# Performance work log

Hardware: AMD Instinct MI355X
Metric: run time of the kernel (lower is better)

## Reference

```python
import jax, jax.numpy as jnp
import numpy as np

B, P, D = 256, 128, 768        # batch, property slots per sample, encoder hidden dim
E = 64                          # num_properties (number of adapter heads)
H = 256                         # adapter_hidden_dim
H2 = H // 2
O = 2                           # output_dim
LN_EPS = 1e-5
RES_W_ADPT, RES_W_BASE = 0.7, 0.3


def setup_inputs() -> dict:
    key = jax.random.key(0)
    ks = jax.random.split(key, 12)
    hidden_states = jax.random.normal(ks[0], (B, P, D), dtype=jnp.float32)
    base_output = jax.random.normal(ks[1], (B, P, O), dtype=jnp.float32)
    properties = jax.random.randint(ks[2], (B, P), 0, E, dtype=jnp.int64)
    mask = (jax.random.uniform(ks[3], (B, P)) > 0.1).astype(jnp.float32)
    # Stacked per-head adapter parameters (LayerNorm + 3 Linears per head)
    ln_g = jnp.ones((E, D), dtype=jnp.float32)
    ln_b = jnp.zeros((E, D), dtype=jnp.float32)
    W1 = jax.random.normal(ks[4], (E, D, H), dtype=jnp.float32) * (1.0 / np.sqrt(D))
    b1 = jnp.zeros((E, H), dtype=jnp.float32)
    W2 = jax.random.normal(ks[5], (E, H, H2), dtype=jnp.float32) * (1.0 / np.sqrt(H))
    b2 = jnp.zeros((E, H2), dtype=jnp.float32)
    W3 = jax.random.normal(ks[6], (E, H2, O), dtype=jnp.float32) * 0.01  # init std=0.01 per source
    b3 = jnp.zeros((E, O), dtype=jnp.float32)
    return {
        "hidden_states": hidden_states, "base_output": base_output,
        "properties": properties, "mask": mask,
        "ln_g": ln_g, "ln_b": ln_b, "W1": W1, "b1": b1,
        "W2": W2, "b2": b2, "W3": W3, "b3": b3,
    }


def reference(hidden_states, base_output, properties, mask,
              ln_g, ln_b, W1, b1, W2, b2, W3, b3):
    b, p, d = hidden_states.shape
    o = W3.shape[-1]
    x = hidden_states.reshape(-1, d)                        # [N, D]
    # LayerNorm statistics are head-independent; only gamma/beta differ per head
    mu = jnp.mean(x, axis=-1, keepdims=True)
    var = jnp.mean((x - mu) ** 2, axis=-1, keepdims=True)
    xhat = (x - mu) * jax.lax.rsqrt(var + LN_EPS)           # [N, D]
    flat_p = properties.reshape(-1)                         # [N]
    flat_m = mask.reshape(-1)                               # [N]

    def body(acc, inp):
        idx, g, bt, w1, bb1, w2, bb2, w3, bb3 = inp
        h = jax.nn.relu((xhat * g + bt) @ w1 + bb1)         # [N, H]  (dropout = identity in eval)
        h = jax.nn.relu(h @ w2 + bb2)                       # [N, H2]
        out = h @ w3 + bb3                                  # [N, O]
        sel = (flat_p == idx) & (flat_m > 0)
        return jnp.where(sel[:, None], out, acc), None

    e = W1.shape[0]
    acc0 = jnp.zeros((b * p, o), dtype=x.dtype)
    acc, _ = jax.lax.scan(
        body, acc0,
        (jnp.arange(e), ln_g, ln_b, W1, b1, W2, b2, W3, b3))
    out = acc.reshape(b, p, o)
    out = RES_W_ADPT * out + RES_W_BASE * base_output       # use_residual=True
    return out * mask[..., None]
```

## Files before the change

kernel.cpp:

```cpp
#include <hip/hip_runtime.h>
#include <stdint.h>

typedef unsigned short u16;
typedef unsigned int   u32;

#define NTOK   32768
#define GD     768
#define GH     256
#define GH2    128
#define GE     64

typedef __bf16 bf16x8 __attribute__((ext_vector_type(8)));
typedef float  f32x4  __attribute__((ext_vector_type(4)));
union Frag { uint4 u; bf16x8 b; };

__device__ __forceinline__ float bf2f(u16 h) {
  union { u32 u; float f; } v; v.u = ((u32)h) << 16; return v.f;
}
__device__ __forceinline__ u16 f2bf(float f) {
  union { float f; u32 u; } v; v.f = f;
  u32 r = (v.u + 0x7fffu + ((v.u >> 16) & 1u)) >> 16;
  return (u16)r;
}

__device__ __forceinline__ void async16(void* lds, const void* g) {
  __builtin_amdgcn_global_load_lds(
      (const __attribute__((address_space(1))) void*)g,
      (__attribute__((address_space(3))) void*)lds, 16, 0, 0);
}

__device__ __forceinline__ int getProp(const int* p32, int t, int is64) {
  return is64 ? p32[2 * t] : p32[t];
}

static const size_t OFF_Y    = 0;
static const size_t OFF_W1T  = 50331648;
static const size_t OFF_W2T  = 75497472;
static const size_t OFF_TOK  = 79691776;
static const size_t OFF_META = 79822848;

__global__ void setup_kernel(const int* __restrict__ prop, const float* __restrict__ mask,
                             u32* __restrict__ outz, int* __restrict__ counts2d,
                             int* __restrict__ cursors_p, int* __restrict__ flagp) {
  __shared__ int h[GE];
  __shared__ int vOr;
  const int b = blockIdx.x;
  const int tid = threadIdx.x;
  outz[b * 512 + tid] = 0u;
  outz[b * 512 + 256 + tid] = 0u;
  if (b < 4) cursors_p[b * 256 + tid] = 0;
  if (tid < GE) h[tid] = 0;
  if (tid == 0) vOr = 0;
  __syncthreads();
  int v = prop[2 * tid + 1] | prop[2 * (tid + 256) + 1];
  if (v) atomicOr(&vOr, 1);
  __syncthreads();
  const int is64 = (vOr == 0) ? 1 : 0;
  if (b == 0 && tid == 0) *flagp = is64;
  const int t = b * 256 + tid;
  if (mask[t] > 0.f) atomicAdd(&h[getProp(prop, t, is64)], 1);
  __syncthreads();
  if (tid < GE) counts2d[b * GE + tid] = h[tid];
}

__global__ void transpose_w1(const float* __restrict__ in, u16* __restrict__ out) {
  __shared__ u16 tl[64][260];
  const int bid = blockIdx.x;
  const int e  = bid / 12, r = bid % 12;
  const int d0 = (r / 4) * 256, h0 = (r % 4) * 64;
  const int tid = threadIdx.x;
  const size_t inMat = (size_t)e * GD * GH;
  const size_t outMat = (size_t)e * GH * GD;
  const int h_l = (tid & 15) * 4, d_l = tid >> 4;
#pragma unroll
  for (int dd = 0; dd < 16; ++dd) {
    const int d = d_l + dd * 16;
    float4 v = *(const float4*)(in + inMat + (size_t)(d0 + d) * GH + h0 + h_l);
    tl[h_l + 0][d] = f2bf(v.x);
    tl[h_l + 1][d] = f2bf(v.y);
    tl[h_l + 2][d] = f2bf(v.z);
    tl[h_l + 3][d] = f2bf(v.w);
  }
  __syncthreads();
  const int wv = tid >> 6, ln = tid & 63;
#pragma unroll
  for (int hh = 0; hh < 16; ++hh) {
    const int h = wv * 16 + hh;
    *(uint2*)(out + outMat + (size_t)(h0 + h) * GD + d0 + ln * 4) =
        *(const uint2*)&tl[h][ln * 4];
  }
}

__global__ void transpose_kernel(const float* __restrict__ in, u16* __restrict__ out,
                                 int R, int C, int tilesC) {
  __shared__ u16 tile[32][33];
  const int tilesPerMat = (R >> 5) * tilesC;
  const int e  = blockIdx.x / tilesPerMat;
  const int t  = blockIdx.x % tilesPerMat;
  const int tr = t / tilesC, tc = t % tilesC;
  const size_t mat = (size_t)e * R * C;
  const int tx = threadIdx.x & 31, ty = threadIdx.x >> 5;
  const int r0 = tr * 32, c0 = tc * 32;
#pragma unroll
  for (int i = 0; i < 32; i += 8)
    tile[ty + i][tx] = f2bf(in[mat + (size_t)(r0 + ty + i) * C + c0 + tx]);
  __syncthreads();
#pragma unroll
  for (int i = 0; i < 32; i += 8)
    out[mat + (size_t)(c0 + ty + i) * R + r0 + tx] = tile[tx][ty + i];
}

__global__ void ln_kernel(const float* __restrict__ hs, const float* __restrict__ g,
                          const float* __restrict__ bta, const int* __restrict__ prop,
                          u16* __restrict__ y, const int* __restrict__ flag) {
  const int wv = threadIdx.x >> 6, ln = threadIdx.x & 63;
  const int t = blockIdx.x * 4 + wv;
  const float* x = hs + (size_t)t * GD;
  float v[12];
  float s = 0.f, sq = 0.f;
#pragma unroll
  for (int c = 0; c < 3; ++c) {
    float4 u = *(const float4*)(x + c * 256 + ln * 4);
    v[c*4+0] = u.x; v[c*4+1] = u.y; v[c*4+2] = u.z; v[c*4+3] = u.w;
    s  += u.x + u.y + u.z + u.w;
    sq += u.x*u.x + u.y*u.y + u.z*u.z + u.w*u.w;
  }
#pragma unroll
  for (int d = 1; d < 64; d <<= 1) { s += __shfl_xor(s, d); sq += __shfl_xor(sq, d); }
  const float mu = s * (1.f / 768.f);
  const float rstd = rsqrtf(sq * (1.f / 768.f) - mu * mu + 1e-5f);
  const int p = getProp(prop, t, *flag);
  const float* gp = g + (size_t)p * GD;
  const float* bp = bta + (size_t)p * GD;
  u16* yp = y + (size_t)t * GD;
#pragma unroll
  for (int c = 0; c < 3; ++c) {
    float4 ug = *(const float4*)(gp + c * 256 + ln * 4);
    float4 ub = *(const float4*)(bp + c * 256 + ln * 4);
    float y0 = (v[c*4+0] - mu) * rstd * ug.x + ub.x;
    float y1 = (v[c*4+1] - mu) * rstd * ug.y + ub.y;
    float y2 = (v[c*4+2] - mu) * rstd * ug.z + ub.z;
    float y3 = (v[c*4+3] - mu) * rstd * ug.w + ub.w;
    uint2 o;
    o.x = (u32)f2bf(y0) | ((u32)f2bf(y1) << 16);
    o.y = (u32)f2bf(y2) | ((u32)f2bf(y3) << 16);
    *(uint2*)(yp + c * 256 + ln * 4) = o;
  }
}

__global__ void scan_kernel(const int* __restrict__ counts2d, int* __restrict__ offsets,
                            int* __restrict__ tileHead, int* __restrict__ tileRow,
                            int* __restrict__ nTilesPtr) {
  const int e = threadIdx.x;
  int c = 0;
  for (int b = 0; b < 128; ++b) c += counts2d[b * GE + e];
  int inc = c;
#pragma unroll
  for (int d = 1; d < 64; d <<= 1) { int n = __shfl_up(inc, d); if (e >= d) inc += n; }
  const int off = inc - c;
  offsets[e] = off;
  if (e == 63) offsets[64] = inc;
  int ntile = (c + 63) >> 6;
  int inct = ntile;
#pragma unroll
  for (int d = 1; d < 64; d <<= 1) { int n = __shfl_up(inct, d); if (e >= d) inct += n; }
  const int tb = inct - ntile;
  for (int j = 0; j < ntile; ++j) { tileHead[tb + j] = e; tileRow[tb + j] = off + j * 64; }
  if (e == 63) *nTilesPtr = inct;
}

__global__ void scatter_kernel(const int* __restrict__ prop, const float* __restrict__ mask,
                               const int* __restrict__ offsets, int* __restrict__ cursors_p,
                               int* __restrict__ tokenIds, const int* __restrict__ flag) {
  __shared__ int h[GE];
  __shared__ int basebin[GE];
  const int tid = threadIdx.x;
  const int t = blockIdx.x * 256 + tid;
  if (tid < GE) h[tid] = 0;
  __syncthreads();
  int p = -1, rank = 0;
  if (mask[t] > 0.f) {
    p = getProp(prop, t, *flag);
    rank = atomicAdd(&h[p], 1);
  }
  __syncthreads();
  if (tid < GE && h[tid] > 0) basebin[tid] = atomicAdd(&cursors_p[tid * 16], h[tid]);
  __syncthreads();
  if (p >= 0) tokenIds[offsets[p] + basebin[p] + rank] = t;
}

__global__ __launch_bounds__(256, 2) void adapter_gemm(
    const u16* __restrict__ y, const u16* __restrict__ w1t, const u16* __restrict__ w2t,
    const float* __restrict__ b1, const float* __restrict__ b2,
    const float* __restrict__ w3, const float* __restrict__ b3,
    const float* __restrict__ base, const float* __restrict__ mask,
    const int* __restrict__ tokenIds, const int* __restrict__ offsets,
    const int* __restrict__ tileHead, const int* __restrict__ tileRow,
    const int* __restrict__ nTilesPtr, float* __restrict__ outp) {
  __shared__ union LU {
    struct { u16 A[2][2048]; u16 B[2][8192]; } s;
    u16 h[17408];
  } uni;
  __shared__ u16 sB2[2][4096];
  __shared__ float sBias1[256];
  __shared__ float sBias2[128];
  __shared__ float sW3[2][128];
  __shared__ float sB3[2];
  __shared__ int   sTok[64];

  const int tid  = threadIdx.x;
  const int wv   = tid >> 6;
  const int ln   = tid & 63;
  const int l15  = tid & 15;
  const int quad = (tid & 63) >> 4;
  const f32x4 vzero = {0.f, 0.f, 0.f, 0.f};
  const int nt = *nTilesPtr;

  for (int tile = blockIdx.x; tile < nt; tile += gridDim.x) {
    __syncthreads();
    const int e  = tileHead[tile];
    const int rs = tileRow[tile];
    const int nRows = min(64, offsets[e + 1] - rs);

    if (tid < 64) sTok[tid] = tokenIds[rs + min(tid, nRows - 1)];
    sBias1[tid] = b1[e * GH + tid];
    if (tid < 128) sBias2[tid] = b2[e * GH2 + tid];
    { const int k = tid >> 1, o = tid & 1; sW3[o][k] = w3[e * GH2 * 2 + k * 2 + o]; }
    if (tid < 2) sB3[tid] = b3[e * 2 + tid];
    __syncthreads();

    const u16* yrow = y + (size_t)sTok[ln] * GD;
    const u16* w1e = w1t + (size_t)e * GH * GD;
    const u16* w2e = w2t + (size_t)e * GH2 * GH;

    f32x4 acc1[4][4];
#pragma unroll
    for (int f = 0; f < 4; ++f)
#pragma unroll
      for (int g = 0; g < 4; ++g) acc1[f][g] = vzero;

    {
      async16(uni.s.A[0] + wv * 512, yrow + wv * 8);
#pragma unroll
      for (int j = 0; j < 4; ++j)
        async16(uni.s.B[0] + wv * 2048 + j * 512,
                w1e + (size_t)(j * 64 + ln) * GD + wv * 8);
    }

    for (int kt = 0; kt < 24; ++kt) {
      __syncthreads();
      if (kt + 1 < 24) {
        const int k0 = (kt + 1) * 32;
        const int par = (kt + 1) & 1;
        async16(uni.s.A[par] + wv * 512, yrow + k0 + wv * 8);
#pragma unroll
        for (int j = 0; j < 4; ++j)
          async16(uni.s.B[par] + wv * 2048 + j * 512,
                  w1e + (size_t)(j * 64 + ln) * GD + k0 + wv * 8);
      }
      const int par = kt & 1;
      Frag fa[4], fb[4];
#pragma unroll
      for (int f = 0; f < 4; ++f)
        fa[f].u = *(const uint4*)&uni.s.A[par][quad * 512 + (f * 16 + l15) * 8];
#pragma unroll
      for (int g = 0; g < 4; ++g)
        fb[g].u = *(const uint4*)&uni.s.B[par][quad * 2048 + (wv * 64 + g * 16 + l15) * 8];
#pragma unroll
      for (int f = 0; f < 4; ++f)
#pragma unroll
        for (int g = 0; g < 4; ++g)
          acc1[f][g] = __builtin_amdgcn_mfma_f32_16x16x32_bf16(fa[f].b, fb[g].b, acc1[f][g], 0, 0, 0);
    }
    __syncthreads();

#pragma unroll
    for (int j = 0; j < 2; ++j)
      async16(sB2[0] + wv * 1024 + j * 512,
              w2e + (size_t)(j * 64 + ln) * GH + wv * 8);

#pragma unroll
    for (int f = 0; f < 4; ++f)
#pragma unroll
      for (int g = 0; g < 4; ++g) {
        const int col = wv * 64 + g * 16 + l15;
        const float bias = sBias1[col];
#pragma unroll
        for (int r = 0; r < 4; ++r) {
          const int row = f * 16 + quad * 4 + r;
          uni.h[row * 264 + col] = f2bf(fmaxf(acc1[f][g][r] + bias, 0.f));
        }
      }

    f32x4 acc2[4][2];
#pragma unroll
    for (int f = 0; f < 4; ++f)
#pragma unroll
      for (int g = 0; g < 2; ++g) acc2[f][g] = vzero;

    for (int kt = 0; kt < 8; ++kt) {
      __syncthreads();
      if (kt + 1 < 8) {
        const int k0 = (kt + 1) * 32;
        const int par = (kt + 1) & 1;
#pragma unroll
        for (int j = 0; j < 2; ++j)
          async16(sB2[par] + wv * 1024 + j * 512,
                  w2e + (size_t)(j * 64 + ln) * GH + k0 + wv * 8);
      }
      const int par = kt & 1;
      Frag fa2[4], fb2[2];
#pragma unroll
      for (int f = 0; f < 4; ++f)
        fa2[f].u = *(const uint4*)&uni.h[(f * 16 + l15) * 264 + kt * 32 + quad * 8];
#pragma unroll
      for (int g = 0; g < 2; ++g)
        fb2[g].u = *(const uint4*)&sB2[par][quad * 1024 + (wv * 32 + g * 16 + l15) * 8];
#pragma unroll
      for (int f = 0; f < 4; ++f)
#pragma unroll
        for (int g = 0; g < 2; ++g)
          acc2[f][g] = __builtin_amdgcn_mfma_f32_16x16x32_bf16(fa2[f].b, fb2[g].b, acc2[f][g], 0, 0, 0);
    }
    __syncthreads();

#pragma unroll
    for (int f = 0; f < 4; ++f)
#pragma unroll
      for (int g = 0; g < 2; ++g) {
        const int col = wv * 32 + g * 16 + l15;
        const float bias = sBias2[col];
#pragma unroll
        for (int r = 0; r < 4; ++r) {
          const int row = f * 16 + quad * 4 + r;
          uni.h[row * 130 + col] = f2bf(fmaxf(acc2[f][g][r] + bias, 0.f));
        }
      }
    __syncthreads();

    const int m = tid >> 1, o = tid & 1;
    if (m < nRows) {
      float a = sB3[o];
      const u16* h2row = &uni.h[m * 130];
#pragma unroll 16
      for (int k = 0; k < 128; ++k) a += bf2f(h2row[k]) * sW3[o][k];
      const int t = sTok[m];
      const float mk = mask[t];
      const float bs = base[t * 2 + o];
      outp[t * 2 + o] = (0.7f * a + 0.3f * bs) * mk;
    }
  }
}

extern "C" void kernel_launch(void* const* d_in, const int* in_sizes, int n_in,
                              void* d_out, int out_size, void* d_ws, size_t ws_size,
                              hipStream_t stream) {
  const float* hs   = (const float*)d_in[0];
  const float* base = (const float*)d_in[1];
  const int*   prop = (const int*)d_in[2];
  const float* mask = (const float*)d_in[3];
  const float* lng  = (const float*)d_in[4];
  const float* lnb  = (const float*)d_in[5];
  const float* W1   = (const float*)d_in[6];
  const float* b1   = (const float*)d_in[7];
  const float* W2   = (const float*)d_in[8];
  const float* b2   = (const float*)d_in[9];
  const float* W3   = (const float*)d_in[10];
  const float* b3   = (const float*)d_in[11];

  char* ws = (char*)d_ws;
  u16* y    = (u16*)(ws + OFF_Y);
  u16* w1t  = (u16*)(ws + OFF_W1T);
  u16* w2t  = (u16*)(ws + OFF_W2T);
  int* tok  = (int*)(ws + OFF_TOK);
  int* meta = (int*)(ws + OFF_META);
  int* counts2d  = meta;
  int* offsets   = meta + 8192;
  int* tileHead  = meta + 8320;
  int* tileRow   = meta + 9344;
  int* nTiles    = meta + 10368;
  int* propFlag  = meta + 10369;
  int* cursors_p = meta + 10432;

  setup_kernel<<<128, 256, 0, stream>>>(prop, mask, (u32*)d_out, counts2d,
                                        cursors_p, propFlag);
  transpose_w1<<<768, 256, 0, stream>>>(W1, w1t);
  transpose_kernel<<<64 * 8 * 4, 256, 0, stream>>>(W2, w2t, GH, GH2, 4);
  ln_kernel<<<NTOK / 4, 256, 0, stream>>>(hs, lng, lnb, prop, y, propFlag);
  scan_kernel<<<1, 64, 0, stream>>>(counts2d, offsets, tileHead, tileRow, nTiles);
  scatter_kernel<<<NTOK / 256, 256, 0, stream>>>(prop, mask, offsets, cursors_p, tok, propFlag);
  adapter_gemm<<<640, 256, 0, stream>>>(y, w1t, w2t, b1, b2, W3, b3, base, mask,
                                        tok, offsets, tileHead, tileRow, nTiles,
                                        (float*)d_out);
}
```

Baseline: 283.0 us.

## Fuse LayerNorm into grouped adapter GEMM and merge prep kernels

Drops the separate LayerNorm pass that wrote a bf16 normalized copy of hidden_states. Each GEMM tile now computes per-token mean and rstd from the fp32 input and normalizes with per-head gamma/beta while staging its A operand into shared memory. The setup and both weight transposes are merged into one launch, and counts2d is stored transposed so the scan can read it with vector loads. This removes a full write and reread of the normalized activations plus several launches. In exchange the GEMM reads fp32 rows twice (once for stats, once for the operand), uses synchronous loads for A instead of async copies, and needs more shared memory, which may lower occupancy.

```diff
diff --git a/kernel.cpp b/kernel.cpp
--- a/kernel.cpp
+++ b/kernel.cpp
@@ -33,118 +33,80 @@
   return is64 ? p32[2 * t] : p32[t];
 }
 
-static const size_t OFF_Y    = 0;
-static const size_t OFF_W1T  = 50331648;
-static const size_t OFF_W2T  = 75497472;
-static const size_t OFF_TOK  = 79691776;
-static const size_t OFF_META = 79822848;
-
-__global__ void setup_kernel(const int* __restrict__ prop, const float* __restrict__ mask,
-                             u32* __restrict__ outz, int* __restrict__ counts2d,
-                             int* __restrict__ cursors_p, int* __restrict__ flagp) {
-  __shared__ int h[GE];
-  __shared__ int vOr;
+static const size_t OFF_W1T  = 0;
+static const size_t OFF_W2T  = 25165824;
+static const size_t OFF_TOK  = 29360128;
+static const size_t OFF_META = 29491200;
+
+__global__ void mega_prep(const int* __restrict__ prop, const float* __restrict__ mask,
+                          const float* __restrict__ W1, const float* __restrict__ W2,
+                          u32* __restrict__ outz, u16* __restrict__ w1t,
+                          u16* __restrict__ w2t, int* __restrict__ counts2d,
+                          int* __restrict__ cursors_p, int* __restrict__ flagp) {
+  __shared__ union SM {
+    struct { int h[GE]; int vOr; } st;
+    u16 w1[64][260];
+    u16 t32[32][33];
+  } sm;
   const int b = blockIdx.x;
   const int tid = threadIdx.x;
-  outz[b * 512 + tid] = 0u;
-  outz[b * 512 + 256 + tid] = 0u;
-  if (b < 4) cursors_p[b * 256 + tid] = 0;
-  if (tid < GE) h[tid] = 0;
-  if (tid == 0) vOr = 0;
-  __syncthreads();
-  int v = prop[2 * tid + 1] | prop[2 * (tid + 256) + 1];
-  if (v) atomicOr(&vOr, 1);
-  __syncthreads();
-  const int is64 = (vOr == 0) ? 1 : 0;
-  if (b == 0 && tid == 0) *flagp = is64;
-  const int t = b * 256 + tid;
-  if (mask[t] > 0.f) atomicAdd(&h[getProp(prop, t, is64)], 1);
-  __syncthreads();
-  if (tid < GE) counts2d[b * GE + tid] = h[tid];
-}
-
-__global__ void transpose_w1(const float* __restrict__ in, u16* __restrict__ out) {
-  __shared__ u16 tl[64][260];
-  const int bid = blockIdx.x;
-  const int e  = bid / 12, r = bid % 12;
-  const int d0 = (r / 4) * 256, h0 = (r % 4) * 64;
-  const int tid = threadIdx.x;
-  const size_t inMat = (size_t)e * GD * GH;
-  const size_t outMat = (size_t)e * GH * GD;
-  const int h_l = (tid & 15) * 4, d_l = tid >> 4;
-#pragma unroll
-  for (int dd = 0; dd < 16; ++dd) {
-    const int d = d_l + dd * 16;
-    float4 v = *(const float4*)(in + inMat + (size_t)(d0 + d) * GH + h0 + h_l);
-    tl[h_l + 0][d] = f2bf(v.x);
-    tl[h_l + 1][d] = f2bf(v.y);
-    tl[h_l + 2][d] = f2bf(v.z);
-    tl[h_l + 3][d] = f2bf(v.w);
-  }
-  __syncthreads();
-  const int wv = tid >> 6, ln = tid & 63;
-#pragma unroll
-  for (int hh = 0; hh < 16; ++hh) {
-    const int h = wv * 16 + hh;
-    *(uint2*)(out + outMat + (size_t)(h0 + h) * GD + d0 + ln * 4) =
-        *(const uint2*)&tl[h][ln * 4];
-  }
-}
-
-__global__ void transpose_kernel(const float* __restrict__ in, u16* __restrict__ out,
-                                 int R, int C, int tilesC) {
-  __shared__ u16 tile[32][33];
-  const int tilesPerMat = (R >> 5) * tilesC;
-  const int e  = blockIdx.x / tilesPerMat;
-  const int t  = blockIdx.x % tilesPerMat;
-  const int tr = t / tilesC, tc = t % tilesC;
-  const size_t mat = (size_t)e * R * C;
-  const int tx = threadIdx.x & 31, ty = threadIdx.x >> 5;
-  const int r0 = tr * 32, c0 = tc * 32;
-#pragma unroll
-  for (int i = 0; i < 32; i += 8)
-    tile[ty + i][tx] = f2bf(in[mat + (size_t)(r0 + ty + i) * C + c0 + tx]);
-  __syncthreads();
-#pragma unroll
-  for (int i = 0; i < 32; i += 8)
-    out[mat + (size_t)(c0 + ty + i) * R + r0 + tx] = tile[tx][ty + i];
-}
-
-__global__ void ln_kernel(const float* __restrict__ hs, const float* __restrict__ g,
-                          const float* __restrict__ bta, const int* __restrict__ prop,
-                          u16* __restrict__ y, const int* __restrict__ flag) {
-  const int wv = threadIdx.x >> 6, ln = threadIdx.x & 63;
-  const int t = blockIdx.x * 4 + wv;
-  const float* x = hs + (size_t)t * GD;
-  float v[12];
-  float s = 0.f, sq = 0.f;
-#pragma unroll
-  for (int c = 0; c < 3; ++c) {
-    float4 u = *(const float4*)(x + c * 256 + ln * 4);
-    v[c*4+0] = u.x; v[c*4+1] = u.y; v[c*4+2] = u.z; v[c*4+3] = u.w;
-    s  += u.x + u.y + u.z + u.w;
-    sq += u.x*u.x + u.y*u.y + u.z*u.z + u.w*u.w;
-  }
-#pragma unroll
-  for (int d = 1; d < 64; d <<= 1) { s += __shfl_xor(s, d); sq += __shfl_xor(sq, d); }
-  const float mu = s * (1.f / 768.f);
-  const float rstd = rsqrtf(sq * (1.f / 768.f) - mu * mu + 1e-5f);
-  const int p = getProp(prop, t, *flag);
-  const float* gp = g + (size_t)p * GD;
-  const float* bp = bta + (size_t)p * GD;
-  u16* yp = y + (size_t)t * GD;
-#pragma unroll
-  for (int c = 0; c < 3; ++c) {
-    float4 ug = *(const float4*)(gp + c * 256 + ln * 4);
-    float4 ub = *(const float4*)(bp + c * 256 + ln * 4);
-    float y0 = (v[c*4+0] - mu) * rstd * ug.x + ub.x;
-    float y1 = (v[c*4+1] - mu) * rstd * ug.y + ub.y;
-    float y2 = (v[c*4+2] - mu) * rstd * ug.z + ub.z;
-    float y3 = (v[c*4+3] - mu) * rstd * ug.w + ub.w;
-    uint2 o;
-    o.x = (u32)f2bf(y0) | ((u32)f2bf(y1) << 16);
-    o.y = (u32)f2bf(y2) | ((u32)f2bf(y3) << 16);
-    *(uint2*)(yp + c * 256 + ln * 4) = o;
+
+  if (b < 128) {
+    outz[b * 512 + tid] = 0u;
+    outz[b * 512 + 256 + tid] = 0u;
+    if (b < 4) cursors_p[b * 256 + tid] = 0;
+    if (tid < GE) sm.st.h[tid] = 0;
+    if (tid == 0) sm.st.vOr = 0;
+    __syncthreads();
+    int v = prop[2 * tid + 1] | prop[2 * (tid + 256) + 1];
+    if (v) atomicOr(&sm.st.vOr, 1);
+    __syncthreads();
+    const int is64 = (sm.st.vOr == 0) ? 1 : 0;
+    if (b == 0 && tid == 0) *flagp = is64;
+    const int t = b * 256 + tid;
+    if (mask[t] > 0.f) atomicAdd(&sm.st.h[getProp(prop, t, is64)], 1);
+    __syncthreads();
+    if (tid < GE) counts2d[tid * 128 + b] = sm.st.h[tid];
+  } else if (b < 896) {
+    const int bid = b - 128;
+    const int e  = bid / 12, r = bid % 12;
+    const int d0 = (r / 4) * 256, h0 = (r % 4) * 64;
+    const size_t inMat = (size_t)e * GD * GH;
+    const size_t outMat = (size_t)e * GH * GD;
+    const int h_l = (tid & 15) * 4, d_l = tid >> 4;
+#pragma unroll
+    for (int dd = 0; dd < 16; ++dd) {
+      const int d = d_l + dd * 16;
+      float4 v = *(const float4*)(W1 + inMat + (size_t)(d0 + d) * GH + h0 + h_l);
+      sm.w1[h_l + 0][d] = f2bf(v.x);
+      sm.w1[h_l + 1][d] = f2bf(v.y);
+      sm.w1[h_l + 2][d] = f2bf(v.z);
+      sm.w1[h_l + 3][d] = f2bf(v.w);
+    }
+    __syncthreads();
+    const int wv = tid >> 6, ln = tid & 63;
+#pragma unroll
+    for (int hh = 0; hh < 16; ++hh) {
+      const int h = wv * 16 + hh;
+      *(uint2*)(w1t + outMat + (size_t)(h0 + h) * GD + d0 + ln * 4) =
+          *(const uint2*)&sm.w1[h][ln * 4];
+    }
+  } else {
+    const int bid = b - 896;
+    const int R = GH, C = GH2, tilesC = 4, tilesPerMat = 32;
+    const int e  = bid / tilesPerMat;
+    const int t  = bid % tilesPerMat;
+    const int tr = t / tilesC, tc = t % tilesC;
+    const size_t mat = (size_t)e * R * C;
+    const int tx = tid & 31, ty = tid >> 5;
+    const int r0 = tr * 32, c0 = tc * 32;
+#pragma unroll
+    for (int i = 0; i < 32; i += 8)
+      sm.t32[ty + i][tx] = f2bf(W2[mat + (size_t)(r0 + ty + i) * C + c0 + tx]);
+    __syncthreads();
+#pragma unroll
+    for (int i = 0; i < 32; i += 8)
+      w2t[mat + (size_t)(c0 + ty + i) * R + r0 + tx] = sm.t32[tx][ty + i];
   }
 }
 
@@ -153,7 +115,9 @@
                             int* __restrict__ nTilesPtr) {
   const int e = threadIdx.x;
   int c = 0;
-  for (int b = 0; b < 128; ++b) c += counts2d[b * GE + e];
+  const int4* p = (const int4*)(counts2d + e * 128);
+#pragma unroll
+  for (int i = 0; i < 32; ++i) { int4 v = p[i]; c += v.x + v.y + v.z + v.w; }
   int inc = c;
 #pragma unroll
   for (int d = 1; d < 64; d <<= 1) { int n = __shfl_up(inc, d); if (e >= d) inc += n; }
@@ -190,7 +154,8 @@
 }
 
 __global__ __launch_bounds__(256, 2) void adapter_gemm(
-    const u16* __restrict__ y, const u16* __restrict__ w1t, const u16* __restrict__ w2t,
+    const float* __restrict__ hs, const float* __restrict__ lng, const float* __restrict__ lnb,
+    const u16* __restrict__ w1t, const u16* __restrict__ w2t,
     const float* __restrict__ b1, const float* __restrict__ b2,
     const float* __restrict__ w3, const float* __restrict__ b3,
     const float* __restrict__ base, const float* __restrict__ mask,
@@ -198,7 +163,14 @@
     const int* __restrict__ tileHead, const int* __restrict__ tileRow,
     const int* __restrict__ nTilesPtr, float* __restrict__ outp) {
   __shared__ union LU {
-    struct { u16 A[2][2048]; u16 B[2][8192]; } s;
+    struct {
+      u16 A[2][2048];
+      u16 B[2][8192];
+      u16 G[768];
+      u16 Bt[768];
+      float mu[64];
+      float rstd[64];
+    } s;
     u16 h[17408];
   } uni;
   __shared__ u16 sB2[2][4096];
@@ -227,11 +199,39 @@
     if (tid < 128) sBias2[tid] = b2[e * GH2 + tid];
     { const int k = tid >> 1, o = tid & 1; sW3[o][k] = w3[e * GH2 * 2 + k * 2 + o]; }
     if (tid < 2) sB3[tid] = b3[e * 2 + tid];
-    __syncthreads();
-
-    const u16* yrow = y + (size_t)sTok[ln] * GD;
+#pragma unroll
+    for (int i = 0; i < 3; ++i) {
+      const int idx = i * 256 + tid;
+      uni.s.G[idx]  = f2bf(lng[e * GD + idx]);
+      uni.s.Bt[idx] = f2bf(lnb[e * GD + idx]);
+    }
+    __syncthreads();
+
+    {
+      const int srow = tid >> 2, sj = tid & 3;
+      const float* xr = hs + (size_t)sTok[srow] * GD;
+      float s = 0.f, sq = 0.f;
+#pragma unroll
+      for (int i = 0; i < 48; ++i) {
+        float4 u = *(const float4*)(xr + i * 16 + sj * 4);
+        s  += u.x + u.y + u.z + u.w;
+        sq += u.x * u.x + u.y * u.y + u.z * u.z + u.w * u.w;
+      }
+      s += __shfl_xor(s, 1);  s += __shfl_xor(s, 2);
+      sq += __shfl_xor(sq, 1); sq += __shfl_xor(sq, 2);
+      if (sj == 0) {
+        const float m = s * (1.f / 768.f);
+        uni.s.mu[srow]   = m;
+        uni.s.rstd[srow] = rsqrtf(sq * (1.f / 768.f) - m * m + 1e-5f);
+      }
+    }
+    __syncthreads();
+
+    const float* xrow = hs + (size_t)sTok[ln] * GD;
     const u16* w1e = w1t + (size_t)e * GH * GD;
     const u16* w2e = w2t + (size_t)e * GH2 * GH;
+    const float lmu = uni.s.mu[ln];
+    const float lrs = uni.s.rstd[ln];
 
     f32x4 acc1[4][4];
 #pragma unroll
@@ -239,26 +239,44 @@
 #pragma unroll
       for (int g = 0; g < 4; ++g) acc1[f][g] = vzero;
 
-    {
-      async16(uni.s.A[0] + wv * 512, yrow + wv * 8);
-#pragma unroll
-      for (int j = 0; j < 4; ++j)
-        async16(uni.s.B[0] + wv * 2048 + j * 512,
-                w1e + (size_t)(j * 64 + ln) * GD + wv * 8);
-    }
+    float4 pa = *(const float4*)(xrow + wv * 8);
+    float4 pb = *(const float4*)(xrow + wv * 8 + 4);
+#pragma unroll
+    for (int j = 0; j < 4; ++j)
+      async16(uni.s.B[0] + wv * 2048 + j * 512,
+              w1e + (size_t)(j * 64 + ln) * GD + wv * 8);
 
     for (int kt = 0; kt < 24; ++kt) {
+      const int par = kt & 1;
+      {
+        const int kb = kt * 32 + wv * 8;
+        const uint4 gv = *(const uint4*)&uni.s.G[kb];
+        const uint4 bv = *(const uint4*)&uni.s.Bt[kb];
+        const float xn0 = (pa.x - lmu) * lrs * bf2f((u16)(gv.x & 0xffff)) + bf2f((u16)(bv.x & 0xffff));
+        const float xn1 = (pa.y - lmu) * lrs * bf2f((u16)(gv.x >> 16))    + bf2f((u16)(bv.x >> 16));
+        const float xn2 = (pa.z - lmu) * lrs * bf2f((u16)(gv.y & 0xffff)) + bf2f((u16)(bv.y & 0xffff));
+        const float xn3 = (pa.w - lmu) * lrs * bf2f((u16)(gv.y >> 16))    + bf2f((u16)(bv.y >> 16));
+        const float xn4 = (pb.x - lmu) * lrs * bf2f((u16)(gv.z & 0xffff)) + bf2f((u16)(bv.z & 0xffff));
+        const float xn5 = (pb.y - lmu) * lrs * bf2f((u16)(gv.z >> 16))    + bf2f((u16)(bv.z >> 16));
+        const float xn6 = (pb.z - lmu) * lrs * bf2f((u16)(gv.w & 0xffff)) + bf2f((u16)(bv.w & 0xffff));
+        const float xn7 = (pb.w - lmu) * lrs * bf2f((u16)(gv.w >> 16))    + bf2f((u16)(bv.w >> 16));
+        uint4 pk;
+        pk.x = (u32)f2bf(xn0) | ((u32)f2bf(xn1) << 16);
+        pk.y = (u32)f2bf(xn2) | ((u32)f2bf(xn3) << 16);
+        pk.z = (u32)f2bf(xn4) | ((u32)f2bf(xn5) << 16);
+        pk.w = (u32)f2bf(xn6) | ((u32)f2bf(xn7) << 16);
+        *(uint4*)&uni.s.A[par][wv * 512 + ln * 8] = pk;
+      }
       __syncthreads();
       if (kt + 1 < 24) {
         const int k0 = (kt + 1) * 32;
-        const int par = (kt + 1) & 1;
-        async16(uni.s.A[par] + wv * 512, yrow + k0 + wv * 8);
+        pa = *(const float4*)(xrow + k0 + wv * 8);
+        pb = *(const float4*)(xrow + k0 + wv * 8 + 4);
 #pragma unroll
         for (int j = 0; j < 4; ++j)
-          async16(uni.s.B[par] + wv * 2048 + j * 512,
+          async16(uni.s.B[(kt + 1) & 1] + wv * 2048 + j * 512,
                   w1e + (size_t)(j * 64 + ln) * GD + k0 + wv * 8);
       }
-      const int par = kt & 1;
       Frag fa[4], fb[4];
 #pragma unroll
       for (int f = 0; f < 4; ++f)
@@ -369,7 +387,6 @@
   const float* b3   = (const float*)d_in[11];
 
   char* ws = (char*)d_ws;
-  u16* y    = (u16*)(ws + OFF_Y);
   u16* w1t  = (u16*)(ws + OFF_W1T);
   u16* w2t  = (u16*)(ws + OFF_W2T);
   int* tok  = (int*)(ws + OFF_TOK);
@@ -382,14 +399,11 @@
   int* propFlag  = meta + 10369;
   int* cursors_p = meta + 10432;
 
-  setup_kernel<<<128, 256, 0, stream>>>(prop, mask, (u32*)d_out, counts2d,
-                                        cursors_p, propFlag);
-  transpose_w1<<<768, 256, 0, stream>>>(W1, w1t);
-  transpose_kernel<<<64 * 8 * 4, 256, 0, stream>>>(W2, w2t, GH, GH2, 4);
-  ln_kernel<<<NTOK / 4, 256, 0, stream>>>(hs, lng, lnb, prop, y, propFlag);
+  mega_prep<<<2944, 256, 0, stream>>>(prop, mask, W1, W2, (u32*)d_out,
+                                      w1t, w2t, counts2d, cursors_p, propFlag);
   scan_kernel<<<1, 64, 0, stream>>>(counts2d, offsets, tileHead, tileRow, nTiles);
   scatter_kernel<<<NTOK / 256, 256, 0, stream>>>(prop, mask, offsets, cursors_p, tok, propFlag);
-  adapter_gemm<<<640, 256, 0, stream>>>(y, w1t, w2t, b1, b2, W3, b3, base, mask,
-                                        tok, offsets, tileHead, tileRow, nTiles,
-                                        (float*)d_out);
-}
+  adapter_gemm<<<640, 256, 0, stream>>>(hs, lng, lnb, w1t, w2t, b1, b2, W3, b3,
+                                        base, mask, tok, offsets, tileHead, tileRow,
+                                        nTiles, (float*)d_out);
+}
```

New measurement: 287.9 us. Within noise of the previous version (+1.7%).
